# Kernel optimization log

Hardware: AMD Instinct MI355X
Metric: run time of the kernel (lower is better)

The kernel has to match this reference:

```python
import jax, jax.numpy as jnp
import numpy as np

EPS = 1e-12

def _l2norm(x):
    n = jnp.sqrt(jnp.sum(x * x, axis=-1, keepdims=True))
    return x / jnp.maximum(n, EPS)

def setup_inputs() -> dict:
    key = jax.random.key(0)
    k1, k2 = jax.random.split(key)
    B, S, H = 32, 256, 768
    return {
        "query_embs": jax.random.normal(k1, (B, S, H), dtype=jnp.float32),
        "key_embs": jax.random.normal(k2, (B, S, H), dtype=jnp.float32),
        "q_mask": jnp.ones((B, S), dtype=jnp.float32),
        "k_mask": jnp.ones((B, S), dtype=jnp.float32),
        "alpha_raw": jnp.asarray(1.0, dtype=jnp.float32),
        "logit_scale": jnp.asarray(0.0, dtype=jnp.float32),  # log(1.0)
    }

def reference(query_embs, key_embs, q_mask, k_mask, alpha_raw, logit_scale):
    # query_embs, key_embs: (B, S, H); masks: (B, S)
    S = query_embs.shape[1]
    q = _l2norm(query_embs)
    k = _l2norm(key_embs)
    # all-pairs token similarity: (B, B, S, T)
    sim = jnp.einsum('ish,jth->ijst', q, k)
    # distance-decay weighting (do_distance=True, exp_decay=True)
    alpha = jax.nn.softplus(alpha_raw)
    pos = jnp.arange(S, dtype=jnp.float32)
    dist = jnp.abs(pos[:, None] - pos[None, :])  # (S, S)
    sim = sim * jnp.exp(-alpha * dist)
    # validity mask: (B, B, S, T)
    valid = (q_mask[:, None, :, None] * k_mask[None, :, None, :]) > 0
    scale = jnp.exp(logit_scale)
    neg_inf = jnp.float32(-jnp.inf)
    logits = jnp.where(valid, scale * sim, neg_inf)
    all_inf = jnp.all(logits == neg_inf, axis=-1, keepdims=True)
    safe_logits = jnp.where(all_inf, 0.0, logits)
    p = jax.nn.softmax(safe_logits, axis=-1)
    p = jnp.where(all_inf, 0.0, p)
    # softmax-weighted key aggregation: (B, B, S, H)
    agg = jnp.einsum('ijst,jth->ijsh', p, k)
    # per-token cosine score, masked mean over query tokens
    scores = jnp.einsum('ish,ijsh->ijs', q, agg) * q_mask[:, None, :]
    denom = jnp.clip(jnp.sum(q_mask, axis=-1, keepdims=True), 1.0, None)
    return jnp.sum(scores, axis=-1) / denom  # (B, B)
```

## Files before the change

kernel.cpp:

```cpp
#include <hip/hip_runtime.h>
#include <cmath>

#define BB 32
#define SS 256
#define HH 768

typedef __attribute__((ext_vector_type(8))) short bfrag8;
typedef __attribute__((ext_vector_type(4))) float accf4;

__device__ __forceinline__ unsigned short f2bf(float x) {
    unsigned int b = __float_as_uint(x);
    return (unsigned short)((b + 0x7FFFu + ((b >> 16) & 1u)) >> 16);
}

__device__ __forceinline__ void gload16(const void* g, void* l) {
    __builtin_amdgcn_global_load_lds((const __attribute__((address_space(1))) void*)g,
                                     (__attribute__((address_space(3))) void*)l, 16, 0, 0);
}


__global__ __launch_bounds__(256)
void zero_kernel(float* __restrict__ Ksum) {
    Ksum[blockIdx.x * 256 + threadIdx.x] = 0.f;
}

__global__ __launch_bounds__(256)
void normcvt_kernel(const float* __restrict__ Q, const float* __restrict__ K,
                    const float* __restrict__ kmask,
                    float* __restrict__ invq, float* __restrict__ invk,
                    unsigned short* __restrict__ qws, unsigned short* __restrict__ kws,
                    float* __restrict__ Ksum) {
    __shared__ float sK[4 * HH];
    const int wave = threadIdx.x >> 6, lane = threadIdx.x & 63;
    const bool isQ = blockIdx.x < 2048;
    const int rr = (blockIdx.x * 4 + wave) & 8191;
    const float4* src4 = isQ ? (const float4*)(Q + (size_t)rr * HH)
                             : (const float4*)(K + (size_t)rr * HH);
    float4 vv[3]; float s = 0.f;
#pragma unroll
    for (int c = 0; c < 3; ++c) {
        vv[c] = src4[lane + 64 * c];
        s += vv[c].x * vv[c].x + vv[c].y * vv[c].y + vv[c].z * vv[c].z + vv[c].w * vv[c].w;
    }
#pragma unroll
    for (int off = 1; off < 64; off <<= 1) s += __shfl_xor(s, off);
    float inv = 1.f / fmaxf(sqrtf(s), 1e-12f);
    if (lane == 0) (isQ ? invq : invk)[rr] = inv;

    const int b = rr >> 8, srow = rr & 255;
    unsigned short* dst = isQ ? qws : kws;
    float m = 0.f;
    if (!isQ) m = (kmask[b * SS + srow] > 0.f) ? 1.f : 0.f;
    const int fp8 = (((((lane & 7) >> 1)) ^ ((srow >> 1) & 3)) << 3) + (lane & 1) * 4;
#pragma unroll
    for (int c = 0; c < 3; ++c) {
        int kc = (lane >> 3) + 8 * c;
        float4 n4;
        n4.x = vv[c].x * inv; n4.y = vv[c].y * inv; n4.z = vv[c].z * inv; n4.w = vv[c].w * inv;
        ushort4 o;
        o.x = f2bf(n4.x); o.y = f2bf(n4.y); o.z = f2bf(n4.z); o.w = f2bf(n4.w);
        *(ushort4*)(dst + (((size_t)b * 24 + kc) * 256 + srow) * 32 + fp8) = o;
        if (!isQ)
            *(float4*)(sK + wave * HH + (lane + 64 * c) * 4) =
                make_float4(n4.x * m, n4.y * m, n4.z * m, n4.w * m);
    }
    if (!isQ) {
        __syncthreads();
        const int j = ((int)blockIdx.x - 2048) >> 6;
        for (int e = threadIdx.x; e < HH; e += 256) {
            float v = sK[e] + sK[HH + e] + sK[2 * HH + e] + sK[3 * HH + e];
            atomicAdd(&Ksum[j * HH + e], v);
        }
    }
}

__global__ __launch_bounds__(256)
void ksum_pack_kernel(const float* __restrict__ Ksum, unsigned short* __restrict__ ksumB) {
    int e = blockIdx.x * 256 + threadIdx.x;
    ksumB[e] = f2bf(Ksum[e]);
}

__global__ __launch_bounds__(256, 4)
void mfma_kernel(const unsigned short* __restrict__ qws, const unsigned short* __restrict__ kws,
                 const float* __restrict__ qmask, const float* __restrict__ kmask,
                 const float* __restrict__ araw_p, const float* __restrict__ lscale_p,
                 const unsigned short* __restrict__ ksumB, float* __restrict__ out) {
    __shared__ short lq[8192];
    __shared__ short lk[8192];
    __shared__ short lKsum[768];
    __shared__ float sKm[256];
    __shared__ float wtab[13];
    __shared__ float sRed[4][2];
    __shared__ float sPart[4];
    __shared__ float sKcnt, sQden;

    const int tid = threadIdx.x;
    const int lane = tid & 63, w = tid >> 6;
    const int quad = lane >> 4, col = lane & 15;
    const int i = blockIdx.x >> 5, j = blockIdx.x & 31;

    const float alpha = log1pf(__expf(araw_p[0]));
    const float scale = __expf(lscale_p[0]);

    float aq = qmask[i * SS + tid];
    float km = kmask[j * SS + tid];
    sKm[tid] = km;
    float c = (km > 0.f) ? 1.f : 0.f;
#pragma unroll
    for (int off = 1; off < 64; off <<= 1) { aq += __shfl_xor(aq, off); c += __shfl_xor(c, off); }
    if (lane == 0) { sRed[w][0] = aq; sRed[w][1] = c; }
    if (tid < 13) wtab[tid] = __expf(-alpha * (float)tid);
    if (tid < 192) ((ushort4*)lKsum)[tid] = ((const ushort4*)(ksumB + (size_t)j * HH))[tid];
    __syncthreads();
    if (tid == 0) {
        sQden = fmaxf(sRed[0][0] + sRed[1][0] + sRed[2][0] + sRed[3][0], 1.f);
        sKcnt = sRed[0][1] + sRed[1][1] + sRed[2][1] + sRed[3][1];
    }

    accf4 acc[4][3];
    accf4 accB[4];
#pragma unroll
    for (int a = 0; a < 4; ++a) {
        accB[a] = (accf4)0.f;
#pragma unroll
        for (int b = 0; b < 3; ++b) acc[a][b] = (accf4)0.f;
    }

    const size_t qb0 = (size_t)i * 24 * 8192;
    const size_t kb0 = (size_t)j * 24 * 8192;
    const int perm8 = ((quad ^ ((col >> 1) & 3)) << 3);

    for (int kc = 0; kc < 24; ++kc) {
        __syncthreads();
        {
            const unsigned short* qs = qws + qb0 + (size_t)kc * 8192 + w * 2048 + lane * 8;
            const unsigned short* ks = kws + kb0 + (size_t)kc * 8192 + w * 2048 + lane * 8;
            unsigned short* lqd = (unsigned short*)lq + w * 2048;
            unsigned short* lkd = (unsigned short*)lk + w * 2048;
#pragma unroll
            for (int n = 0; n < 4; ++n) {
                gload16(qs + n * 512, lqd + n * 512);
                gload16(ks + n * 512, lkd + n * 512);
            }
        }
        __syncthreads();

        const bfrag8 kfrag = *(const bfrag8*)(lKsum + kc * 32 + quad * 8);
        bfrag8 bfr[6];
#pragma unroll
        for (int u = 0; u < 6; ++u) {
            int tb = 4 * w - 1 + u;
            if (tb >= 0 && tb <= 15)
                bfr[u] = *(const bfrag8*)(lk + (size_t)(tb * 16 + col) * 32 + perm8);
        }
#pragma unroll
        for (int sbl = 0; sbl < 4; ++sbl) {
            bfrag8 af = *(const bfrag8*)(lq + (size_t)((4 * w + sbl) * 16 + col) * 32 + perm8);
            accB[sbl] = __builtin_amdgcn_mfma_f32_16x16x32_bf16(af, kfrag, accB[sbl], 0, 0, 0);
#pragma unroll
            for (int dtb = 0; dtb < 3; ++dtb) {
                int tb = 4 * w + sbl - 1 + dtb;
                if (tb >= 0 && tb <= 15)
                    acc[sbl][dtb] = __builtin_amdgcn_mfma_f32_16x16x32_bf16(
                        af, bfr[sbl + dtb], acc[sbl][dtb], 0, 0, 0);
            }
        }
    }

    __syncthreads();
    const float kcnt = sKcnt;
    float part = 0.f;
#pragma unroll
    for (int sbl = 0; sbl < 4; ++sbl) {
        const int sbase = (4 * w + sbl) * 16 + quad * 4;
        float ns[4] = {0.f, 0.f, 0.f, 0.f}, ds[4] = {0.f, 0.f, 0.f, 0.f};
#pragma unroll
        for (int dtb = 0; dtb < 3; ++dtb) {
            int tb = 4 * w + sbl - 1 + dtb;
            if (tb < 0 || tb > 15) continue;
            int t = tb * 16 + col;
            float kmv = sKm[t];
#pragma unroll
            for (int reg = 0; reg < 4; ++reg) {
                int st = sbase + reg;
                int d = t - st;
                bool ok = (d >= -11) && (d <= 12) && (kmv > 0.f);
                int idx = d < 0 ? -d : d;
                idx = ok ? idx : 0;
                float raw = acc[sbl][dtb][reg];
                float e = ok ? expm1f(scale * raw * wtab[idx]) : 0.f;
                ns[reg] = fmaf(e, raw, ns[reg]);
                ds[reg] += e;
            }
        }
#pragma unroll
        for (int off = 1; off < 16; off <<= 1) {
#pragma unroll
            for (int reg = 0; reg < 4; ++reg) {
                ns[reg] += __shfl_xor(ns[reg], off);
                ds[reg] += __shfl_xor(ds[reg], off);
            }
        }
        if (col == 0) {
#pragma unroll
            for (int reg = 0; reg < 4; ++reg) {
                int st = sbase + reg;
                float qm = qmask[i * SS + st];
                float bse = accB[sbl][reg];
                float dtot = ds[reg] + kcnt;
                float v = (qm > 0.f && kcnt > 0.f) ? qm * (ns[reg] + bse) / dtot : 0.f;
                part += v;
            }
        }
    }
    part += __shfl_xor(part, 16);
    part += __shfl_xor(part, 32);
    if (lane == 0) sPart[w] = part;
    __syncthreads();
    if (tid == 0) out[i * BB + j] = (sPart[0] + sPart[1] + sPart[2] + sPart[3]) / sQden;
}


extern "C" void kernel_launch(void* const* d_in, const int* in_sizes, int n_in,
                              void* d_out, int out_size, void* d_ws, size_t ws_size,
                              hipStream_t stream) {
    const float* Q      = (const float*)d_in[0];
    const float* K      = (const float*)d_in[1];
    const float* qmask  = (const float*)d_in[2];
    const float* kmask  = (const float*)d_in[3];
    const float* araw   = (const float*)d_in[4];
    const float* lscale = (const float*)d_in[5];
    float* outp = (float*)d_out;

    float* invq  = (float*)d_ws;
    float* invk  = invq + 8192;
    float* Ksum  = invk + 8192;
    unsigned short* ksumB = (unsigned short*)(Ksum + 24576);
    unsigned short* qws = ksumB + 24576;
    unsigned short* kws = qws + 6291456;

    zero_kernel<<<96, 256, 0, stream>>>(Ksum);
    normcvt_kernel<<<4096, 256, 0, stream>>>(Q, K, kmask, invq, invk, qws, kws, Ksum);
    ksum_pack_kernel<<<96, 256, 0, stream>>>(Ksum, ksumB);
    mfma_kernel<<<1024, 256, 0, stream>>>(qws, kws, qmask, kmask, araw, lscale, ksumB, outp);
}
```

Before: 150.1 us.

## Register-prefetch next tile, fold ksum packing into mfma kernel

Measured after the change: 163.2 us. 8.7% more time.

```diff
diff --git a/kernel.cpp b/kernel.cpp
--- a/kernel.cpp
+++ b/kernel.cpp
@@ -11,11 +11,6 @@
 __device__ __forceinline__ unsigned short f2bf(float x) {
     unsigned int b = __float_as_uint(x);
     return (unsigned short)((b + 0x7FFFu + ((b >> 16) & 1u)) >> 16);
-}
-
-__device__ __forceinline__ void gload16(const void* g, void* l) {
-    __builtin_amdgcn_global_load_lds((const __attribute__((address_space(1))) void*)g,
-                                     (__attribute__((address_space(3))) void*)l, 16, 0, 0);
 }
 
 
@@ -74,17 +69,11 @@
     }
 }
 
-__global__ __launch_bounds__(256)
-void ksum_pack_kernel(const float* __restrict__ Ksum, unsigned short* __restrict__ ksumB) {
-    int e = blockIdx.x * 256 + threadIdx.x;
-    ksumB[e] = f2bf(Ksum[e]);
-}
-
-__global__ __launch_bounds__(256, 4)
+__global__ __launch_bounds__(256, 3)
 void mfma_kernel(const unsigned short* __restrict__ qws, const unsigned short* __restrict__ kws,
                  const float* __restrict__ qmask, const float* __restrict__ kmask,
                  const float* __restrict__ araw_p, const float* __restrict__ lscale_p,
-                 const unsigned short* __restrict__ ksumB, float* __restrict__ out) {
+                 const float* __restrict__ Ksum, float* __restrict__ out) {
     __shared__ short lq[8192];
     __shared__ short lk[8192];
     __shared__ short lKsum[768];
@@ -110,7 +99,12 @@
     for (int off = 1; off < 64; off <<= 1) { aq += __shfl_xor(aq, off); c += __shfl_xor(c, off); }
     if (lane == 0) { sRed[w][0] = aq; sRed[w][1] = c; }
     if (tid < 13) wtab[tid] = __expf(-alpha * (float)tid);
-    if (tid < 192) ((ushort4*)lKsum)[tid] = ((const ushort4*)(ksumB + (size_t)j * HH))[tid];
+    if (tid < 192) {
+        float4 kv = ((const float4*)(Ksum + (size_t)j * HH))[tid];
+        ushort4 o;
+        o.x = f2bf(kv.x); o.y = f2bf(kv.y); o.z = f2bf(kv.z); o.w = f2bf(kv.w);
+        ((ushort4*)lKsum)[tid] = o;
+    }
     __syncthreads();
     if (tid == 0) {
         sQden = fmaxf(sRed[0][0] + sRed[1][0] + sRed[2][0] + sRed[3][0], 1.f);
@@ -129,18 +123,31 @@
     const size_t qb0 = (size_t)i * 24 * 8192;
     const size_t kb0 = (size_t)j * 24 * 8192;
     const int perm8 = ((quad ^ ((col >> 1) & 3)) << 3);
+    const unsigned short* qsrc = qws + qb0 + w * 2048 + lane * 8;
+    const unsigned short* ksrc = kws + kb0 + w * 2048 + lane * 8;
+    unsigned short* lqd = (unsigned short*)lq + w * 2048 + lane * 8;
+    unsigned short* lkd = (unsigned short*)lk + w * 2048 + lane * 8;
+
+    bfrag8 pq[4], pk[4];
+#pragma unroll
+    for (int n = 0; n < 4; ++n) {
+        pq[n] = *(const bfrag8*)(qsrc + n * 512);
+        pk[n] = *(const bfrag8*)(ksrc + n * 512);
+    }
 
     for (int kc = 0; kc < 24; ++kc) {
         __syncthreads();
+#pragma unroll
+        for (int n = 0; n < 4; ++n) {
+            *(bfrag8*)(lqd + n * 512) = pq[n];
+            *(bfrag8*)(lkd + n * 512) = pk[n];
+        }
         {
-            const unsigned short* qs = qws + qb0 + (size_t)kc * 8192 + w * 2048 + lane * 8;
-            const unsigned short* ks = kws + kb0 + (size_t)kc * 8192 + w * 2048 + lane * 8;
-            unsigned short* lqd = (unsigned short*)lq + w * 2048;
-            unsigned short* lkd = (unsigned short*)lk + w * 2048;
+            const size_t noff = (size_t)((kc < 23) ? kc + 1 : 23) * 8192;
 #pragma unroll
             for (int n = 0; n < 4; ++n) {
-                gload16(qs + n * 512, lqd + n * 512);
-                gload16(ks + n * 512, lkd + n * 512);
+                pq[n] = *(const bfrag8*)(qsrc + noff + n * 512);
+                pk[n] = *(const bfrag8*)(ksrc + noff + n * 512);
             }
         }
         __syncthreads();
@@ -235,12 +242,10 @@
     float* invq  = (float*)d_ws;
     float* invk  = invq + 8192;
     float* Ksum  = invk + 8192;
-    unsigned short* ksumB = (unsigned short*)(Ksum + 24576);
-    unsigned short* qws = ksumB + 24576;
+    unsigned short* qws = (unsigned short*)(Ksum + 24576);
     unsigned short* kws = qws + 6291456;
 
     zero_kernel<<<96, 256, 0, stream>>>(Ksum);
     normcvt_kernel<<<4096, 256, 0, stream>>>(Q, K, kmask, invq, invk, qws, kws, Ksum);
-    ksum_pack_kernel<<<96, 256, 0, stream>>>(Ksum, ksumB);
-    mfma_kernel<<<1024, 256, 0, stream>>>(qws, kws, qmask, kmask, araw, lscale, ksumB, outp);
-}
+    mfma_kernel<<<1024, 256, 0, stream>>>(qws, kws, qmask, kmask, araw, lscale, Ksum, outp);
+}
```
